# Performance work log

Hardware: AMD Instinct MI355X
Metric: run time of the kernel (lower is better)

Reference implementation:

```python
import jax, jax.numpy as jnp
import numpy as np

H = 8   # num_heads
K = 2   # num_timescales (hard-coded in module)


def _apply_rope(x, cos, sin):
    # x: [B,T,H,D]; cos/sin: [1,T,1,D/2]; interleaved even/odd pairs
    xp = x.reshape(*x.shape[:-1], -1, 2)
    xr, xi = xp[..., 0], xp[..., 1]
    rr = xr * cos - xi * sin
    ri = xr * sin + xi * cos
    return jnp.stack([rr, ri], axis=-1).reshape(x.shape)


def setup_inputs() -> dict:
    key = jax.random.key(0)
    ks = jax.random.split(key, 11)
    B, T, C = 4, 2048, 1024
    HK = H * K
    s = 0.02  # xavier-ish scale
    return {
        'x': jax.random.normal(ks[0], (B, T, C), jnp.float32),
        'mask': jnp.ones((B, T), jnp.int32),
        'Wq': jax.random.normal(ks[1], (C, C), jnp.float32) * s,
        'Wk': jax.random.normal(ks[2], (C, C), jnp.float32) * s,
        'Wv': jax.random.normal(ks[3], (C, C), jnp.float32) * s,
        'Wb': jax.random.normal(ks[4], (C, HK), jnp.float32) * s,
        'bb': jax.random.normal(ks[5], (HK,), jnp.float32) * 0.5 + 2.0,
        'Wm': jax.random.normal(ks[6], (C, HK), jnp.float32) * s,
        'bm': jax.random.normal(ks[7], (HK,), jnp.float32) * 0.1,
        'Wo': jax.random.normal(ks[8], (C, C), jnp.float32) * s,
        'bo': jnp.zeros((C,), jnp.float32),
    }


def reference(x, mask, Wq, Wk, Wv, Wb, bb, Wm, bm, Wo, bo):
    B, T, C = x.shape
    D = C // H
    q = (x @ Wq).reshape(B, T, H, D)
    k = (x @ Wk).reshape(B, T, H, D)
    v = (x @ Wv).reshape(B, T, H, D)

    # RoPE cache
    inv_freq = 1.0 / (10000.0 ** (jnp.arange(0, D, 2, dtype=jnp.float32) / D))
    freqs = jnp.arange(T, dtype=jnp.float32)[:, None] * inv_freq[None, :]  # [T,D/2]
    cos = jnp.cos(freqs)[None, :, None, :].astype(x.dtype)
    sin = jnp.sin(freqs)[None, :, None, :].astype(x.dtype)
    q = _apply_rope(q, cos, sin)
    k = _apply_rope(k, cos, sin)

    beta = jax.nn.sigmoid((x @ Wb + bb).reshape(B, T, H, K))  # [B,T,H,K]
    mix = jax.nn.softmax((x @ Wm + bm).reshape(B, T, H, K), axis=-1)

    def step(S, ins):
        # S: [B,H,K,D,D]
        q_t, k_t, v_t, b_t, m_t, mk = ins  # [B,H,D],[B,H,D],[B,H,D],[B,H,K],[B,H,K],[B]
        outer = jnp.einsum('bhd,bhe->bhde', k_t, v_t)          # [B,H,D,D]
        S_new = b_t[..., None, None] * S + outer[:, :, None]   # [B,H,K,D,D]
        S = jnp.where(mk[:, None, None, None, None] > 0, S_new, S)
        y_k = jnp.einsum('bhd,bhkde->bhke', q_t, S)            # [B,H,K,D]
        y_t = jnp.sum(y_k * m_t[..., None], axis=2)            # [B,H,D]
        y_t = jnp.where(mk[:, None, None] > 0, y_t, jnp.zeros_like(y_t))
        return S, y_t

    S0 = jnp.zeros((B, H, K, D, D), x.dtype)
    xs = (jnp.swapaxes(q, 0, 1), jnp.swapaxes(k, 0, 1), jnp.swapaxes(v, 0, 1),
          jnp.swapaxes(beta, 0, 1), jnp.swapaxes(mix, 0, 1), mask.T)
    _, ys = jax.lax.scan(step, S0, xs)           # ys: [T,B,H,D]
    y = jnp.swapaxes(ys, 0, 1).reshape(B, T, C)
    return y @ Wo + bo
```

## Files before the change

### kernel.cpp

```cpp
#include <hip/hip_runtime.h>

typedef __attribute__((ext_vector_type(4))) float f32x4;
typedef __attribute__((ext_vector_type(8))) __bf16 bf16x8;

#define T_DIM 2048
#define B_DIM 4
#define C_DIM 1024
#define H_N 8
#define D_H 128
#define M_ROWS 8192
#define MC ((size_t)M_ROWS * C_DIM)
#define LCH 64
#define NCH (T_DIM / LCH)
#define CHSZ (128 * 128)
#define SWE(r) ((((r) ^ ((r) >> 3)) & 7) << 3)

#define GLDS16(g, l) __builtin_amdgcn_global_load_lds( \
    (const __attribute__((address_space(1))) void*)(g), \
    (__attribute__((address_space(3))) void*)(l), 16, 0, 0)

__global__ void small_prep_k(float2* __restrict__ tab,
                             const float* __restrict__ Wb,
                             const float* __restrict__ Wm,
                             __bf16* __restrict__ WbmT) {
    int bid = blockIdx.x;
    if (bid < 512) {
        int idx = bid * 256 + threadIdx.x;
        int t = idx >> 6, i = idx & 63;
        float freq = expf(-(2.0f * (float)i / 128.0f) * 9.210340371976184f);
        float a = (float)t * freq;
        tab[idx] = make_float2(cosf(a), sinf(a));
    } else {
        int n = bid - 512;
        int col = n & 15;
        const float* W = (n < 16) ? Wb : Wm;
        for (int k = threadIdx.x; k < C_DIM; k += 256)
            WbmT[(size_t)n * C_DIM + k] = (__bf16)W[(size_t)k * 16 + col];
    }
}

__global__ __launch_bounds__(256) void cvt_x_k(const float* __restrict__ in,
                                               __bf16* __restrict__ out) {
    int i = blockIdx.x * 256 + threadIdx.x;
    f32x4 a = ((const f32x4*)in)[i * 2];
    f32x4 b = ((const f32x4*)in)[i * 2 + 1];
    bf16x8 o;
    o[0] = (__bf16)a.x; o[1] = (__bf16)a.y; o[2] = (__bf16)a.z; o[3] = (__bf16)a.w;
    o[4] = (__bf16)b.x; o[5] = (__bf16)b.y; o[6] = (__bf16)b.z; o[7] = (__bf16)b.w;
    ((bf16x8*)out)[i] = o;
}

__global__ __launch_bounds__(256) void wtrans_k(
    const float* __restrict__ W0, const float* __restrict__ W1,
    const float* __restrict__ W2, const float* __restrict__ W3,
    __bf16* __restrict__ out) {
    const float* W = blockIdx.z == 0 ? W0 : blockIdx.z == 1 ? W1 :
                     blockIdx.z == 2 ? W2 : W3;
    __bf16* o = out + (size_t)blockIdx.z * C_DIM * C_DIM;
    __shared__ float t[64][65];
    int tid = threadIdx.x;
    int r0 = blockIdx.y * 64, c0 = blockIdx.x * 64;
    #pragma unroll
    for (int it = 0; it < 4; ++it) {
        int idx = it * 256 + tid;
        int r = idx >> 4, c4 = (idx & 15) * 4;
        f32x4 v = *(const f32x4*)(W + (size_t)(r0 + r) * C_DIM + c0 + c4);
        t[r][c4] = v.x; t[r][c4 + 1] = v.y; t[r][c4 + 2] = v.z; t[r][c4 + 3] = v.w;
    }
    __syncthreads();
    #pragma unroll
    for (int it = 0; it < 2; ++it) {
        int idx = it * 256 + tid;
        int n = idx >> 3, k8 = (idx & 7) * 8;
        bf16x8 ov;
        #pragma unroll
        for (int j = 0; j < 8; ++j) ov[j] = (__bf16)t[k8 + j][n];
        *(bf16x8*)(o + (size_t)(c0 + n) * C_DIM + r0 + k8) = ov;
    }
}

__global__ __launch_bounds__(256) void betamix_mfma(
    const __bf16* __restrict__ xb, const __bf16* __restrict__ WbmT,
    const float* __restrict__ bb, const float* __restrict__ bm,
    float* __restrict__ beta, float* __restrict__ mix) {
    __shared__ __bf16 As[2][32 * 64];

    int tid = threadIdx.x;
    int w = tid >> 6, lane = tid & 63;
    int lr = lane & 15, lg = lane >> 4;
    int ifr = w >> 1, j = w & 1;
    int rows0 = blockIdx.x * 32;

    int srow = tid >> 3;
    int sg = (tid & 7) ^ (srow & 7);
    size_t aoff = (size_t)(rows0 + srow) * C_DIM + sg * 8;
    int ldso = w * 64 * 16;

    f32x4 acc = {};
    const __bf16* Wrow = WbmT + (size_t)(j * 16 + lr) * C_DIM;

    GLDS16(xb + aoff, (char*)As[0] + ldso);
    asm volatile("s_waitcnt vmcnt(0)" ::: "memory");
    __syncthreads();

    for (int t = 0; t < 16; ++t) {
        int cur = t & 1;
        if (t < 15) GLDS16(xb + aoff + (t + 1) * 64, (char*)As[cur ^ 1] + ldso);
        #pragma unroll
        for (int ss = 0; ss < 2; ++ss) {
            int ar = ifr * 16 + lr;
            bf16x8 af = *(const bf16x8*)((char*)As[cur] + ar * 128 + (((ss * 4 + lg) ^ (ar & 7)) << 4));
            bf16x8 bf = *(const bf16x8*)(Wrow + t * 64 + ss * 32 + lg * 8);
            acc = __builtin_amdgcn_mfma_f32_16x16x32_bf16(af, bf, acc, 0, 0, 0);
        }
        asm volatile("s_waitcnt vmcnt(0)" ::: "memory");
        __syncthreads();
    }

    float bias = (j ? bm : bb)[lr];
    #pragma unroll
    for (int r = 0; r < 4; ++r) {
        int row = rows0 + ifr * 16 + lg * 4 + r;
        float v = acc[r] + bias;
        if (j == 0) {
            beta[(size_t)row * 16 + lr] = 1.f / (1.f + expf(-v));
        } else {
            float other = __shfl_xor(v, 1);
            float mx = fmaxf(v, other);
            float e = expf(v - mx), eo = expf(other - mx);
            mix[(size_t)row * 16 + lr] = e / (e + eo);
        }
    }
}

__global__ __launch_bounds__(256) void decay_k(
    const float* __restrict__ beta, const float* __restrict__ mixp,
    const int* __restrict__ mask,
    float* __restrict__ wvm, float* __restrict__ rcm,
    float* __restrict__ qsc, float* __restrict__ cumLg) {
    int gw = blockIdx.x * 4 + (threadIdx.x >> 6);
    int s = threadIdx.x & 63;
    int scan = gw >> 5, c = gw & 31;
    int b = scan >> 4, hh = scan & 15;
    size_t row = (size_t)b * T_DIM + c * LCH + s;
    int mk = mask[row];
    float mf = mk ? 1.f : 0.f;
    float bt = mk ? beta[row * 16 + hh] : 1.f;
    float mx = mk ? mixp[row * 16 + hh] : 0.f;
    float cum = bt;
    #pragma unroll
    for (int off = 1; off < 64; off <<= 1) {
        float p = __shfl(cum, (s >= off) ? s - off : 0);
        if (s >= off) cum *= p;
    }
    float cl = __shfl(cum, 63);
    size_t o = (size_t)scan * T_DIM + c * LCH + s;
    wvm[o] = mf * cl / cum;
    rcm[o] = mf / cum;
    qsc[o] = mf * mx * cum;
    if (s == 63) cumLg[scan * NCH + c] = cl;
}

template<bool ROPE, bool OUTF32>
__global__ __launch_bounds__(256) void gemm_bt(
    const __bf16* __restrict__ A, const __bf16* __restrict__ BT,
    void* __restrict__ Cp, int M, int N, int K,
    const float2* __restrict__ rope_tab, const float* __restrict__ bias) {
    __shared__ __bf16 As[2][128 * 64];
    __shared__ __bf16 Bs[2][128 * 64];

    int tid = threadIdx.x;
    int nTN = N >> 7;
    int cpx = gridDim.x >> 3;
    int bid = ((int)blockIdx.x & 7) * cpx + ((int)blockIdx.x >> 3);
    int bm = bid / nTN, bn = bid % nTN;
    int m_base = bm << 7, n_base = bn << 7;
    int w = tid >> 6, lane = tid & 63;
    int lr = lane & 15, lg = lane >> 4;
    int wm = (w >> 1) * 64, wn = (w & 1) * 64;

    size_t aoff[4], boff[4];
    int ldso[4];
    #pragma unroll
    for (int it = 0; it < 4; ++it) {
        int gi = it * 256 + tid;
        int row = gi >> 3;
        int g = (gi & 7) ^ (row & 7);
        aoff[it] = (size_t)(m_base + row) * K + g * 8;
        boff[it] = (size_t)(n_base + row) * K + g * 8;
        ldso[it] = (it * 256 + w * 64) * 16;
    }

#define STAGE_G(bufi, k0)                                                   \
    _Pragma("unroll")                                                       \
    for (int it = 0; it < 4; ++it) {                                        \
        GLDS16(A + aoff[it] + (k0), (char*)As[bufi] + ldso[it]);            \
        GLDS16(BT + boff[it] + (k0), (char*)Bs[bufi] + ldso[it]);           \
    }

    f32x4 acc[4][4] = {};

    STAGE_G(0, 0);
    asm volatile("s_waitcnt vmcnt(0)" ::: "memory");
    __syncthreads();

    int nt = K >> 6;
    for (int t = 0; t < nt; ++t) {
        int cur = t & 1;
        if (t + 1 < nt) STAGE_G(cur ^ 1, (t + 1) * 64);
        #pragma unroll
        for (int ss = 0; ss < 2; ++ss) {
            bf16x8 af[4], bfr[4];
            #pragma unroll
            for (int i = 0; i < 4; ++i) {
                int ar = wm + i * 16 + lr;
                af[i] = *(const bf16x8*)((char*)As[cur] + ar * 128 + (((ss * 4 + lg) ^ (ar & 7)) << 4));
                int br = wn + i * 16 + lr;
                bfr[i] = *(const bf16x8*)((char*)Bs[cur] + br * 128 + (((ss * 4 + lg) ^ (br & 7)) << 4));
            }
            #pragma unroll
            for (int i = 0; i < 4; ++i)
                #pragma unroll
                for (int j = 0; j < 4; ++j)
                    acc[i][j] = __builtin_amdgcn_mfma_f32_16x16x32_bf16(af[i], bfr[j], acc[i][j], 0, 0, 0);
        }
        asm volatile("s_waitcnt vmcnt(0)" ::: "memory");
        __syncthreads();
    }
#undef STAGE_G

    #pragma unroll
    for (int i = 0; i < 4; ++i) {
        #pragma unroll
        for (int j = 0; j < 4; ++j) {
            #pragma unroll
            for (int r = 0; r < 4; ++r) {
                int grow = m_base + wm + i * 16 + (lg << 2) + r;
                int gcol = n_base + wn + j * 16 + lr;
                float val = acc[i][j][r];
                if (ROPE) {
                    float partner = __shfl_xor(val, 1);
                    int t = grow & (T_DIM - 1);
                    int ii = (gcol & 127) >> 1;
                    float2 cs = rope_tab[t * 64 + ii];
                    val = (gcol & 1) ? (partner * cs.y + val * cs.x)
                                     : (val * cs.x - partner * cs.y);
                }
                if (bias) val += bias[gcol];
                size_t idx = (size_t)grow * N + gcol;
                if (OUTF32) ((float*)Cp)[idx] = val;
                else        ((__bf16*)Cp)[idx] = (__bf16)val;
            }
        }
    }
}

__global__ __launch_bounds__(256) void chunk_sum_k(
    const __bf16* __restrict__ kg, const __bf16* __restrict__ vg,
    const float* __restrict__ wvm, __bf16* __restrict__ BT) {
    __shared__ __bf16 KT[128 * 64];
    __shared__ __bf16 VT[128 * 64];

    int tid = threadIdx.x;
    int c = blockIdx.x, kk = blockIdx.y, bh = blockIdx.z;
    int b = bh >> 3, h = bh & 7;
    int scan = bh * 2 + kk;
    size_t rowb = (size_t)b * T_DIM + c * LCH;
    size_t wb = (size_t)scan * T_DIM + c * LCH;

    #pragma unroll
    for (int it = 0; it < 4; ++it) {
        int f = tid + it * 256;
        int s = f >> 4, c8 = (f & 15) * 8;
        size_t g = (rowb + s) * C_DIM + h * D_H + c8;
        bf16x8 kv = *(const bf16x8*)(kg + g);
        bf16x8 vv = *(const bf16x8*)(vg + g);
        float ws_ = wvm[wb + s];
        #pragma unroll
        for (int j = 0; j < 8; ++j) {
            int d = c8 + j;
            KT[d * 64 + (s ^ SWE(d))] = (__bf16)(ws_ * (float)kv[j]);
            VT[d * 64 + (s ^ SWE(d))] = vv[j];
        }
    }
    __syncthreads();

    int w = tid >> 6, l = tid & 63;
    int lr = l & 15, lg = l >> 4;
    f32x4 acc[2][8] = {};
    #pragma unroll
    for (int kt = 0; kt < 2; ++kt) {
        int col = kt * 32 + lg * 8;
        bf16x8 aV[2], bK[8];
        #pragma unroll
        for (int et = 0; et < 2; ++et) {
            int e = w * 32 + et * 16 + lr;
            aV[et] = *(const bf16x8*)&VT[e * 64 + (col ^ SWE(e))];
        }
        #pragma unroll
        for (int dt = 0; dt < 8; ++dt) {
            int d = dt * 16 + lr;
            bK[dt] = *(const bf16x8*)&KT[d * 64 + (col ^ SWE(d))];
        }
        #pragma unroll
        for (int et = 0; et < 2; ++et)
            #pragma unroll
            for (int dt = 0; dt < 8; ++dt)
                acc[et][dt] = __builtin_amdgcn_mfma_f32_16x16x32_bf16(aV[et], bK[dt], acc[et][dt], 0, 0, 0);
    }

    __bf16* bout = BT + ((size_t)scan * NCH + c) * CHSZ;
    #pragma unroll
    for (int et = 0; et < 2; ++et)
        #pragma unroll
        for (int dt = 0; dt < 8; ++dt)
            #pragma unroll
            for (int r = 0; r < 4; ++r) {
                int e = w * 32 + et * 16 + lg * 4 + r;
                bout[e * 128 + dt * 16 + lr] = (__bf16)acc[et][dt][r];
            }
}

__global__ __launch_bounds__(256) void chunk_scan_k(
    __bf16* __restrict__ BT, const float* __restrict__ cumLg) {
    int bid = blockIdx.x;
    int scan = bid >> 3, part = bid & 7;
    int tid = threadIdx.x;
    int e = part * 16 + (tid >> 4);
    int d0 = (tid & 15) * 8;
    __bf16* base = BT + (size_t)scan * NCH * CHSZ + e * 128 + d0;
    const float* cl = cumLg + scan * NCH;
    float acc[8] = {};
    for (int c = 0; c < NCH; ++c) {
        bf16x8 bv = *(const bf16x8*)(base + (size_t)c * CHSZ);
        float g = cl[c];
        bf16x8 so;
        #pragma unroll
        for (int j = 0; j < 8; ++j) so[j] = (__bf16)acc[j];
        *(bf16x8*)(base + (size_t)c * CHSZ) = so;
        #pragma unroll
        for (int j = 0; j < 8; ++j) acc[j] = g * acc[j] + (float)bv[j];
    }
}

__global__ __launch_bounds__(256, 3) void chunk_out_k(
    const __bf16* __restrict__ qg, const __bf16* __restrict__ kg,
    const __bf16* __restrict__ vg, const __bf16* __restrict__ ST,
    const float* __restrict__ rcm, const float* __restrict__ qscg,
    __bf16* __restrict__ yg) {
    __shared__ __bf16 STs[2][64 * 128];
    __shared__ __bf16 VT[64 * 64];
    __shared__ __bf16 Ps[64 * 72];
    __shared__ float rcumf[2][64], qscf[2][64];

    int tid = threadIdx.x;
    int c = blockIdx.x, eh = blockIdx.y, bh = blockIdx.z;
    int b = bh >> 3, h = bh & 7;
    int e0 = eh * 64;
    size_t rowb = (size_t)b * T_DIM + c * LCH;
    int w = tid >> 6, l = tid & 63;
    int lr = l & 15, lg = l >> 4;

    {
        const __bf16* stb = ST + ((size_t)(bh * 2) * NCH + c) * CHSZ + (size_t)e0 * 128;
        int r = tid >> 4, gran = tid & 15;
        size_t goff = (size_t)r * 128 + ((gran ^ (r & 7)) * 8);
        #pragma unroll
        for (int kk = 0; kk < 2; ++kk) {
            const __bf16* sp = stb + (size_t)kk * NCH * CHSZ;
            #pragma unroll
            for (int it = 0; it < 4; ++it) {
                GLDS16(sp + goff + (size_t)it * 16 * 128,
                       (char*)STs[kk] + (it * 256 + w * 64) * 16);
            }
        }
    }

    if (tid < 128) {
        int s = tid & 63, kk = tid >> 6;
        size_t o = (size_t)(bh * 2 + kk) * T_DIM + c * LCH + s;
        rcumf[kk][s] = rcm[o];
        qscf[kk][s] = qscg[o];
    }

    bf16x8 vreg[2];
    #pragma unroll
    for (int it = 0; it < 2; ++it) {
        int f = tid + it * 256;
        int s = f >> 3, c8 = (f & 7) * 8;
        vreg[it] = *(const bf16x8*)(vg + (rowb + s) * C_DIM + h * D_H + e0 + c8);
    }

    const __bf16* qrow = qg + (rowb + w * 16 + lr) * C_DIM + h * D_H;
    bf16x8 aQ[4];
    #pragma unroll
    for (int kt = 0; kt < 4; ++kt)
        aQ[kt] = *(const bf16x8*)(qrow + kt * 32 + lg * 8);

    const __bf16* kbase = kg + rowb * C_DIM + h * D_H;
    bf16x8 bkreg[16];
    #pragma unroll
    for (int st = 0; st < 4; ++st)
        #pragma unroll
        for (int kt = 0; kt < 4; ++kt)
            bkreg[st * 4 + kt] = *(const bf16x8*)(kbase + (size_t)(st * 16 + lr) * C_DIM + kt * 32 + lg * 8);

    #pragma unroll
    for (int it = 0; it < 2; ++it) {
        int f = tid + it * 256;
        int s = f >> 3, c8 = (f & 7) * 8;
        #pragma unroll
        for (int j = 0; j < 8; ++j) {
            int el = c8 + j;
            VT[el * 64 + (s ^ SWE(el))] = vreg[it][j];
        }
    }

    f32x4 Praw[4];
    #pragma unroll
    for (int st = 0; st < 4; ++st) {
        f32x4 p = {};
        #pragma unroll
        for (int kt = 0; kt < 4; ++kt)
            p = __builtin_amdgcn_mfma_f32_16x16x32_bf16(aQ[kt], bkreg[st * 4 + kt], p, 0, 0, 0);
        Praw[st] = p;
    }

    asm volatile("s_waitcnt vmcnt(0)" ::: "memory");
    __syncthreads();

    f32x4 yA[4] = {};
    #pragma unroll
    for (int kk = 0; kk < 2; ++kk) {
        #pragma unroll
        for (int st = 0; st < 4; ++st) {
            #pragma unroll
            for (int r = 0; r < 4; ++r) {
                int tl = w * 16 + lg * 4 + r;
                int sc = st * 16 + lr;
                float pv = (sc <= tl) ? Praw[st][r] * rcumf[kk][sc] * qscf[kk][tl] : 0.f;
                Ps[tl * 72 + sc] = (__bf16)pv;
            }
        }
        bf16x8 aP[2];
        #pragma unroll
        for (int k2 = 0; k2 < 2; ++k2)
            aP[k2] = *(const bf16x8*)&Ps[(w * 16 + lr) * 72 + k2 * 32 + lg * 8];

        __builtin_amdgcn_s_setprio(1);
        #pragma unroll
        for (int et = 0; et < 4; ++et) {
            int el = et * 16 + lr;
            f32x4 ys = {};
            #pragma unroll
            for (int kt = 0; kt < 4; ++kt) {
                bf16x8 bs = *(const bf16x8*)((char*)STs[kk] + el * 256 + (((kt * 4 + lg) ^ (el & 7)) << 4));
                ys = __builtin_amdgcn_mfma_f32_16x16x32_bf16(aQ[kt], bs, ys, 0, 0, 0);
            }
            f32x4 yp = {};
            #pragma unroll
            for (int k2 = 0; k2 < 2; ++k2) {
                bf16x8 bv = *(const bf16x8*)&VT[el * 64 + ((k2 * 32 + lg * 8) ^ SWE(el))];
                yp = __builtin_amdgcn_mfma_f32_16x16x32_bf16(aP[k2], bv, yp, 0, 0, 0);
            }
            #pragma unroll
            for (int r = 0; r < 4; ++r)
                yA[et][r] += ys[r] * qscf[kk][w * 16 + lg * 4 + r] + yp[r];
        }
        __builtin_amdgcn_s_setprio(0);
    }
    #pragma unroll
    for (int et = 0; et < 4; ++et)
        #pragma unroll
        for (int r = 0; r < 4; ++r) {
            size_t row = rowb + w * 16 + lg * 4 + r;
            yg[row * C_DIM + h * D_H + e0 + et * 16 + lr] = (__bf16)yA[et][r];
        }
}

extern "C" void kernel_launch(void* const* d_in, const int* in_sizes, int n_in,
                              void* d_out, int out_size, void* d_ws, size_t ws_size,
                              hipStream_t stream) {
    const float* x    = (const float*)d_in[0];
    const int*   mask = (const int*)d_in[1];
    const float* Wq   = (const float*)d_in[2];
    const float* Wk   = (const float*)d_in[3];
    const float* Wv   = (const float*)d_in[4];
    const float* Wb   = (const float*)d_in[5];
    const float* bb   = (const float*)d_in[6];
    const float* Wm   = (const float*)d_in[7];
    const float* bm   = (const float*)d_in[8];
    const float* Wo   = (const float*)d_in[9];
    const float* bo   = (const float*)d_in[10];
    float* out = (float*)d_out;

    __bf16* q    = (__bf16*)d_ws;
    __bf16* k    = q + MC;
    __bf16* v    = k + MC;
    __bf16* xb   = v + MC;
    __bf16* WT   = xb + MC;
    __bf16* BT   = WT + (size_t)4 * C_DIM * C_DIM;
    float* beta  = (float*)(BT + (size_t)64 * NCH * CHSZ);
    float* mixb  = beta + M_ROWS * 16;
    float* cumL  = mixb + M_ROWS * 16;
    float* wvm   = cumL + 64 * NCH;
    float* rcm   = wvm + (size_t)64 * T_DIM;
    float* qscg  = rcm + (size_t)64 * T_DIM;
    float2* rope = (float2*)(qscg + (size_t)64 * T_DIM);
    __bf16* WbmT = (__bf16*)(rope + T_DIM * 64);
    __bf16* ysum = xb;

    small_prep_k<<<dim3(544), dim3(256), 0, stream>>>(rope, Wb, Wm, WbmT);
    cvt_x_k<<<dim3(MC / 8 / 256), dim3(256), 0, stream>>>(x, xb);
    wtrans_k<<<dim3(16, 16, 4), dim3(256), 0, stream>>>(Wq, Wk, Wv, Wo, WT);
    betamix_mfma<<<dim3(M_ROWS / 32), dim3(256), 0, stream>>>(xb, WbmT, bb, bm, beta, mixb);
    decay_k<<<dim3(512), dim3(256), 0, stream>>>(beta, mixb, mask, wvm, rcm, qscg, cumL);

    const size_t CC = (size_t)C_DIM * C_DIM;
    dim3 ggrid((M_ROWS / 128) * (C_DIM / 128));
    gemm_bt<true,  false><<<ggrid, dim3(256), 0, stream>>>(xb, WT,          q,   M_ROWS, C_DIM, C_DIM, rope, nullptr);
    gemm_bt<true,  false><<<ggrid, dim3(256), 0, stream>>>(xb, WT + CC,     k,   M_ROWS, C_DIM, C_DIM, rope, nullptr);
    gemm_bt<false, false><<<ggrid, dim3(256), 0, stream>>>(xb, WT + 2 * CC, v,   M_ROWS, C_DIM, C_DIM, nullptr, nullptr);

    chunk_sum_k<<<dim3(NCH, 2, 32), dim3(256), 0, stream>>>(k, v, wvm, BT);
    chunk_scan_k<<<dim3(512), dim3(256), 0, stream>>>(BT, cumL);
    chunk_out_k<<<dim3(NCH, 2, 32), dim3(256), 0, stream>>>(q, k, v, BT, rcm, qscg, ysum);

    gemm_bt<false, true><<<ggrid, dim3(256), 0, stream>>>(ysum, WT + 3 * CC, out, M_ROWS, C_DIM, C_DIM, nullptr, bo);
}
```

Measured before the change: 227.1 us.

## Fuse Q/K/V projections into one GEMM launch with XCD-aware tile mapping

Replaces three separate projection GEMM launches with a single kernel over a concatenated 3072-wide weight, so x is shared across all three projections. Tiles are assigned so that each XCD owns a block of M rows, which is meant to improve L2 reuse of the A tiles. RoPE is applied only to the first two output buffers. The new kernel uses single-buffered LDS with two barriers per k-step instead of the double-buffered pipeline, which may expose load latency. It assumes q, k and v are laid out contiguously at MC spacing.

Measured after the change: 220.8 us. 1.03x faster.

```diff
diff --git a/kernel.cpp b/kernel.cpp
--- a/kernel.cpp
+++ b/kernel.cpp
@@ -161,11 +161,91 @@
     if (s == 63) cumLg[scan * NCH + c] = cl;
 }
 
-template<bool ROPE, bool OUTF32>
+__global__ __launch_bounds__(256) void gemm_qkv(
+    const __bf16* __restrict__ A, const __bf16* __restrict__ BT,
+    __bf16* __restrict__ outq, const float2* __restrict__ rope_tab) {
+    __shared__ __bf16 As[128 * 64];
+    __shared__ __bf16 Bs[128 * 64];
+    const int K = C_DIM;
+
+    int tid = threadIdx.x;
+    int xcd = blockIdx.x & 7, lid = blockIdx.x >> 3;
+    int g = lid >> 6, u = lid & 63;
+    int bm = xcd * 8 + (u >> 3), bn = g * 8 + (u & 7);
+    int m_base = bm << 7, n_base = bn << 7;
+    int w = tid >> 6, lane = tid & 63;
+    int lr = lane & 15, lg = lane >> 4;
+    int wm = (w >> 1) * 64, wn = (w & 1) * 64;
+
+    size_t aoff[4], boff[4];
+    int ldso[4];
+    #pragma unroll
+    for (int it = 0; it < 4; ++it) {
+        int gi = it * 256 + tid;
+        int row = gi >> 3;
+        int gr = (gi & 7) ^ (row & 7);
+        aoff[it] = (size_t)(m_base + row) * K + gr * 8;
+        boff[it] = (size_t)(n_base + row) * K + gr * 8;
+        ldso[it] = (it * 256 + w * 64) * 16;
+    }
+
+    f32x4 acc[4][4] = {};
+
+    for (int k0 = 0; k0 < K; k0 += 64) {
+        __syncthreads();
+        #pragma unroll
+        for (int it = 0; it < 4; ++it) {
+            GLDS16(A + aoff[it] + k0, (char*)As + ldso[it]);
+            GLDS16(BT + boff[it] + k0, (char*)Bs + ldso[it]);
+        }
+        __syncthreads();
+        #pragma unroll
+        for (int ss = 0; ss < 2; ++ss) {
+            bf16x8 af[4], bfr[4];
+            #pragma unroll
+            for (int i = 0; i < 4; ++i) {
+                int ar = wm + i * 16 + lr;
+                af[i] = *(const bf16x8*)((char*)As + ar * 128 + (((ss * 4 + lg) ^ (ar & 7)) << 4));
+                int br = wn + i * 16 + lr;
+                bfr[i] = *(const bf16x8*)((char*)Bs + br * 128 + (((ss * 4 + lg) ^ (br & 7)) << 4));
+            }
+            #pragma unroll
+            for (int i = 0; i < 4; ++i)
+                #pragma unroll
+                for (int j = 0; j < 4; ++j)
+                    acc[i][j] = __builtin_amdgcn_mfma_f32_16x16x32_bf16(af[i], bfr[j], acc[i][j], 0, 0, 0);
+        }
+    }
+
+    #pragma unroll
+    for (int i = 0; i < 4; ++i) {
+        #pragma unroll
+        for (int j = 0; j < 4; ++j) {
+            #pragma unroll
+            for (int r = 0; r < 4; ++r) {
+                int grow = m_base + wm + i * 16 + (lg << 2) + r;
+                int gcol = n_base + wn + j * 16 + lr;
+                float val = acc[i][j][r];
+                int buf = gcol >> 10;
+                int col = gcol & 1023;
+                if (buf < 2) {
+                    float partner = __shfl_xor(val, 1);
+                    int t = grow & (T_DIM - 1);
+                    int ii = (col & 127) >> 1;
+                    float2 cs = rope_tab[t * 64 + ii];
+                    val = (col & 1) ? (partner * cs.y + val * cs.x)
+                                    : (val * cs.x - partner * cs.y);
+                }
+                outq[(size_t)buf * MC + (size_t)grow * C_DIM + col] = (__bf16)val;
+            }
+        }
+    }
+}
+
 __global__ __launch_bounds__(256) void gemm_bt(
     const __bf16* __restrict__ A, const __bf16* __restrict__ BT,
-    void* __restrict__ Cp, int M, int N, int K,
-    const float2* __restrict__ rope_tab, const float* __restrict__ bias) {
+    float* __restrict__ Cp, int M, int N, int K,
+    const float* __restrict__ bias) {
     __shared__ __bf16 As[2][128 * 64];
     __shared__ __bf16 Bs[2][128 * 64];
 
@@ -237,19 +317,8 @@
             for (int r = 0; r < 4; ++r) {
                 int grow = m_base + wm + i * 16 + (lg << 2) + r;
                 int gcol = n_base + wn + j * 16 + lr;
-                float val = acc[i][j][r];
-                if (ROPE) {
-                    float partner = __shfl_xor(val, 1);
-                    int t = grow & (T_DIM - 1);
-                    int ii = (gcol & 127) >> 1;
-                    float2 cs = rope_tab[t * 64 + ii];
-                    val = (gcol & 1) ? (partner * cs.y + val * cs.x)
-                                     : (val * cs.x - partner * cs.y);
-                }
-                if (bias) val += bias[gcol];
-                size_t idx = (size_t)grow * N + gcol;
-                if (OUTF32) ((float*)Cp)[idx] = val;
-                else        ((__bf16*)Cp)[idx] = (__bf16)val;
+                float val = acc[i][j][r] + bias[gcol];
+                Cp[(size_t)grow * N + gcol] = val;
             }
         }
     }
@@ -517,14 +586,12 @@
     decay_k<<<dim3(512), dim3(256), 0, stream>>>(beta, mixb, mask, wvm, rcm, qscg, cumL);
 
     const size_t CC = (size_t)C_DIM * C_DIM;
-    dim3 ggrid((M_ROWS / 128) * (C_DIM / 128));
-    gemm_bt<true,  false><<<ggrid, dim3(256), 0, stream>>>(xb, WT,          q,   M_ROWS, C_DIM, C_DIM, rope, nullptr);
-    gemm_bt<true,  false><<<ggrid, dim3(256), 0, stream>>>(xb, WT + CC,     k,   M_ROWS, C_DIM, C_DIM, rope, nullptr);
-    gemm_bt<false, false><<<ggrid, dim3(256), 0, stream>>>(xb, WT + 2 * CC, v,   M_ROWS, C_DIM, C_DIM, nullptr, nullptr);
+    gemm_qkv<<<dim3(1536), dim3(256), 0, stream>>>(xb, WT, q, rope);
 
     chunk_sum_k<<<dim3(NCH, 2, 32), dim3(256), 0, stream>>>(k, v, wvm, BT);
     chunk_scan_k<<<dim3(512), dim3(256), 0, stream>>>(BT, cumL);
     chunk_out_k<<<dim3(NCH, 2, 32), dim3(256), 0, stream>>>(q, k, v, BT, rcm, qscg, ysum);
 
-    gemm_bt<false, true><<<ggrid, dim3(256), 0, stream>>>(ysum, WT + 3 * CC, out, M_ROWS, C_DIM, C_DIM, nullptr, bo);
-}
+    gemm_bt<<<dim3((M_ROWS / 128) * (C_DIM / 128)), dim3(256), 0, stream>>>(
+        ysum, WT + 3 * CC, out, M_ROWS, C_DIM, C_DIM, bo);
+}
```
